# Performance work log

Hardware: AMD Instinct MI355X
Metric: run time of the kernel (lower is better)

Reference implementation:

```python
import jax, jax.numpy as jnp
import numpy as np

B, T, C, H = 2, 2048, 1024, 16
D = C // H  # head_dim = 64


def setup_inputs() -> dict:
    key = jax.random.key(0)
    ks = jax.random.split(key, 5)
    s = 1.0 / np.sqrt(C)
    return {
        "x": jax.random.normal(ks[0], (B, T, C), jnp.float32),
        "Wq": jax.random.normal(ks[1], (C, C), jnp.float32) * s,
        "bq": jnp.zeros((C,), jnp.float32),
        "Wk": jax.random.normal(ks[2], (C, C), jnp.float32) * s,
        "bk": jnp.zeros((C,), jnp.float32),
        "Wv": jax.random.normal(ks[3], (C, C), jnp.float32) * s,
        "bv": jnp.zeros((C,), jnp.float32),
        "Wo": jax.random.normal(ks[4], (C, C), jnp.float32) * s,
        "bo": jnp.zeros((C,), jnp.float32),
    }


def reference(x, Wq, bq, Wk, bk, Wv, bv, Wo, bo):
    Bx, Tx, Cx = x.shape
    # torch Linear: y = x @ W.T + b
    q = (x @ Wq.T + bq).reshape(Bx, Tx, H, D).transpose(0, 2, 1, 3)  # [B,H,T,D]
    k = (x @ Wk.T + bk).reshape(Bx, Tx, H, D).transpose(0, 2, 1, 3)
    v = (x @ Wv.T + bv).reshape(Bx, Tx, H, D).transpose(0, 2, 1, 3)
    att = jnp.einsum("bhqd,bhkd->bhqk", q, k) / np.sqrt(D).astype(np.float32)
    mask = jnp.tril(jnp.ones((Tx, Tx), bool))  # causal mask [T,T]
    att = jnp.where(mask, att, -jnp.inf)
    att = jax.nn.softmax(att, axis=-1)
    out = jnp.einsum("bhqk,bhkd->bhqd", att, v)
    out = out.transpose(0, 2, 1, 3).reshape(Bx, Tx, Cx)
    return out @ Wo.T + bo
```

## Files before the change

### kernel.cpp

```cpp
#include <hip/hip_runtime.h>
#include <hip/hip_bf16.h>

#define B_ 2
#define T_ 2048
#define C_ 1024
#define H_ 16
#define D_ 64

typedef unsigned short u16;
typedef __bf16 bf16x8 __attribute__((ext_vector_type(8)));
typedef float floatx4 __attribute__((ext_vector_type(4)));

__device__ __forceinline__ float bf2f(u16 u) {
  union { unsigned int i; float f; } x; x.i = ((unsigned int)u) << 16; return x.f;
}
__device__ __forceinline__ u16 f2bf(float f) {
  union { float f; unsigned int i; } x; x.f = f;
  unsigned int r = x.i + 0x7fffu + ((x.i >> 16) & 1u);
  return (u16)(r >> 16);
}

__device__ __forceinline__ void gld16(void* lds, const void* g) {
  __builtin_amdgcn_global_load_lds(
      (const __attribute__((address_space(1))) unsigned int*)g,
      (__attribute__((address_space(3))) unsigned int*)lds, 16, 0, 0);
}

#define NXF4 1048576
#define NWF4 262144

__global__ __launch_bounds__(256) void cvt_all(
    const float* __restrict__ x,  const float* __restrict__ Wq,
    const float* __restrict__ Wk, const float* __restrict__ Wv,
    const float* __restrict__ Wo, u16* __restrict__ dst_base)
{
  const int i = blockIdx.x * 256 + threadIdx.x;
  const float* src; size_t off;
  if (i < NXF4)               { src = x;  off = i; }
  else if (i < NXF4 + NWF4)   { src = Wq; off = i - NXF4; }
  else if (i < NXF4 + 2*NWF4) { src = Wk; off = i - (NXF4 + NWF4); }
  else if (i < NXF4 + 3*NWF4) { src = Wv; off = i - (NXF4 + 2*NWF4); }
  else                        { src = Wo; off = i - (NXF4 + 3*NWF4); }
  float4 f = ((const float4*)src)[off];
  ushort4 o;
  o.x = f2bf(f.x); o.y = f2bf(f.y); o.z = f2bf(f.z); o.w = f2bf(f.w);
  ((ushort4*)dst_base)[i] = o;
}

#define QSCALE 0.1803368801111f

#define MFMA16(MH, NH, BREG)                                                  \
  do {                                                                        \
    __builtin_amdgcn_s_setprio(1);                                            \
    _Pragma("unroll")                                                         \
    for (int f = 0; f < 4; ++f) {                                             \
      _Pragma("unroll")                                                       \
      for (int g = 0; g < 2; ++g) {                                           \
        acc[(MH)*4 + f][(NH)*2 + g] = __builtin_amdgcn_mfma_f32_16x16x32_bf16(\
            a[f][0], BREG[g][0], acc[(MH)*4 + f][(NH)*2 + g], 0, 0, 0);       \
        acc[(MH)*4 + f][(NH)*2 + g] = __builtin_amdgcn_mfma_f32_16x16x32_bf16(\
            a[f][1], BREG[g][1], acc[(MH)*4 + f][(NH)*2 + g], 0, 0, 0);       \
      }                                                                       \
    }                                                                         \
    __builtin_amdgcn_s_setprio(0);                                            \
  } while (0)

#define PBAR()                                                \
  do {                                                        \
    asm volatile("" ::: "memory");                            \
    __builtin_amdgcn_s_barrier();                             \
    asm volatile("s_waitcnt lgkmcnt(0)" ::: "memory");        \
  } while (0)

#define EBAR()                                                \
  do {                                                        \
    asm volatile("" ::: "memory");                            \
    __builtin_amdgcn_s_barrier();                             \
    asm volatile("" ::: "memory");                            \
  } while (0)

__global__ __launch_bounds__(512, 2) void gemm_qkv8(
    const u16* __restrict__ X, const u16* __restrict__ Wb,
    const float* __restrict__ b0, const float* __restrict__ b1,
    const float* __restrict__ b2,
    u16* __restrict__ Yq, u16* __restrict__ Yk, u16* __restrict__ Yv)
{
  __shared__ __align__(16) u16 L[65536];

  const int tid  = threadIdx.x;
  const int lane = tid & 63;
  const int m16  = lane & 15;
  const int q4   = lane >> 4;
  const int wv   = tid >> 6;
  const int wm   = wv >> 2;
  const int wn   = wv & 3;

  const int bid = blockIdx.x;
  const int xcd = bid & 7;
  const int idx = bid >> 3;
  const int bx  = (xcd & 3) * 4 + (idx & 3);
  const int by  = (xcd >> 2) * 6 + (idx >> 2);

  const u16* Abase  = X  + (size_t)bx * 256 * C_;
  const u16* Bbase  = Wb + (size_t)by * 256 * C_;
  const u16* A1base = Abase + (size_t)128 * C_;
  const u16* B1base = Bbase + (size_t)128 * C_;

  const int s0 = tid,       r0 = s0 >> 3;
  const int s1 = tid + 512, r1 = s1 >> 3;
  const int k0a = ((s0 & 7) ^ (r0 & 7)) * 8;
  const int k1a = ((s1 & 7) ^ (r1 & 7)) * 8;

#define STAGE(dsthalf, srcrows, kofs)                                         \
  do {                                                                        \
    gld16(&(dsthalf)[s0 * 8], (srcrows) + (size_t)r0 * C_ + (kofs) + k0a);    \
    gld16(&(dsthalf)[s1 * 8], (srcrows) + (size_t)r1 * C_ + (kofs) + k1a);    \
  } while (0)

  u16* buf0 = L;
  u16* buf1 = L + 32768;

  STAGE(buf0 + 16384, Bbase, 0);
  STAGE(buf0,         Abase, 0);
  STAGE(buf0 + 24576, B1base, 0);
  STAGE(buf0 + 8192,  A1base, 0);
  STAGE(buf1 + 16384, Bbase, 64);
  STAGE(buf1,         Abase, 64);
  asm volatile("s_waitcnt vmcnt(4)" ::: "memory");
  __builtin_amdgcn_s_barrier();
  asm volatile("" ::: "memory");

  floatx4 acc[8][4] = {};

  const int a0off = m16 * 64 + ((q4      ^ (lane & 7)) * 8);
  const int a1off = m16 * 64 + (((q4 + 4) ^ (lane & 7)) * 8);
  const int bro   = (wn & 1) * 4096;

  for (int i = 0; i < 16; ++i) {
    u16* buf  = (i & 1) ? buf1 : buf0;
    u16* bufn = (i & 1) ? buf0 : buf1;
    const u16* Ah = buf + wm * 8192;
    const u16* Bh = buf + 16384 + (wn >> 1) * 8192;
    const bool p1 = (i + 1) < 16;
    const bool p2 = (i + 2) < 16;
    const int  k1 = (i + 1) * 64;
    const int  k2 = (i + 2) * 64;

    bf16x8 a[4][2], bA[2][2], bB[2][2];

#pragma unroll
    for (int f = 0; f < 4; ++f) {
      a[f][0] = *(const bf16x8*)&Ah[f * 1024 + a0off];
      a[f][1] = *(const bf16x8*)&Ah[f * 1024 + a1off];
    }
#pragma unroll
    for (int g = 0; g < 2; ++g) {
      bA[g][0] = *(const bf16x8*)&Bh[bro + g * 1024 + a0off];
      bA[g][1] = *(const bf16x8*)&Bh[bro + g * 1024 + a1off];
    }
    if (p1) STAGE(bufn + 24576, B1base, k1);
    PBAR();
    MFMA16(0, 0, bA);
    EBAR();

#pragma unroll
    for (int g = 0; g < 2; ++g) {
      bB[g][0] = *(const bf16x8*)&Bh[bro + 2048 + g * 1024 + a0off];
      bB[g][1] = *(const bf16x8*)&Bh[bro + 2048 + g * 1024 + a1off];
    }
    if (p1) STAGE(bufn + 8192, A1base, k1);
    PBAR();
    MFMA16(0, 1, bB);
    EBAR();

#pragma unroll
    for (int f = 0; f < 4; ++f) {
      a[f][0] = *(const bf16x8*)&Ah[4096 + f * 1024 + a0off];
      a[f][1] = *(const bf16x8*)&Ah[4096 + f * 1024 + a1off];
    }
    if (p2) STAGE(buf + 16384, Bbase, k2);
    PBAR();
    MFMA16(1, 1, bB);
    EBAR();

    if (p2) STAGE(buf, Abase, k2);
    PBAR();
    MFMA16(1, 0, bA);
    asm volatile("" ::: "memory");
    if (p2) asm volatile("s_waitcnt vmcnt(4)" ::: "memory");
    else    asm volatile("s_waitcnt vmcnt(0)" ::: "memory");
    __builtin_amdgcn_s_barrier();
    asm volatile("" ::: "memory");
  }

  const int z    = by >> 2;
  const int nloc = (by & 3) * 256 + wn * 64;
  const float* bias = (z == 0) ? b0 : (z == 1) ? b1 : b2;
  const int mbase = bx * 256 + wm * 128 + q4 * 4;

  if (z == 2) {
#pragma unroll
    for (int nf = 0; nf < 4; ++nf) {
      const int nz = nloc + nf * 16 + m16;
      const float bv = bias[nz];
      const int h = nz >> 6, d = nz & (D_ - 1);
#pragma unroll
      for (int mf = 0; mf < 8; ++mf) {
        const int m  = mbase + mf * 16;
        const int bb = m >> 11, t = m & (T_ - 1);
        ushort4 pk;
        pk.x = f2bf(acc[mf][nf][0] + bv);
        pk.y = f2bf(acc[mf][nf][1] + bv);
        pk.z = f2bf(acc[mf][nf][2] + bv);
        pk.w = f2bf(acc[mf][nf][3] + bv);
        *(ushort4*)&Yv[(((size_t)bb * H_ + h) * D_ + d) * T_ + t] = pk;
      }
    }
  } else {
    u16* Y = z ? Yk : Yq;
    const float sc = z ? 1.0f : QSCALE;
#pragma unroll
    for (int nf = 0; nf < 4; ++nf) {
      const int nz = nloc + nf * 16 + m16;
      const float bv = bias[nz];
      const int h = nz >> 6, d = nz & (D_ - 1);
#pragma unroll
      for (int mf = 0; mf < 8; ++mf) {
        const int m  = mbase + mf * 16;
        const int bb = m >> 11, tq = m & (T_ - 1);
#pragma unroll
        for (int r = 0; r < 4; ++r) {
          Y[(((size_t)bb * H_ + h) * T_ + (tq + r)) * D_ + d] =
              f2bf((acc[mf][nf][r] + bv) * sc);
        }
      }
    }
  }
}

__global__ __launch_bounds__(256) void gemm_out(
    const u16* __restrict__ X, const u16* __restrict__ W,
    const float* __restrict__ bias, float* __restrict__ Yf)
{
  const int K = C_, N = C_;
  __shared__ __align__(16) u16 As[128 * 32];
  __shared__ __align__(16) u16 Bs[64 * 32];

  const int tid  = threadIdx.x;
  const int wv   = tid >> 6;
  const int lane = tid & 63;
  const int mcol = lane & 15;
  const int quad = lane >> 4;
  const int wr = wv >> 1, wc = wv & 1;
  const int m0 = blockIdx.x * 128;
  const int n0 = blockIdx.y * 64;

  const int srow = tid >> 2;
  const int scol = (tid & 3) * 8;
  const u16* xp0 = X + (size_t)(m0 + srow) * K + scol;
  const u16* xp1 = xp0 + (size_t)64 * K;
  const u16* wp  = W + (size_t)(n0 + srow) * K + scol;

  floatx4 acc[4][2] = {};

  for (int k0 = 0; k0 < K; k0 += 32) {
    gld16(&As[tid * 8],        xp0 + k0);
    gld16(&As[2048 + tid * 8], xp1 + k0);
    gld16(&Bs[tid * 8],        wp + k0);
    __syncthreads();

    bf16x8 a[4], b[2];
#pragma unroll
    for (int rf = 0; rf < 4; ++rf)
      a[rf] = *(const bf16x8*)&As[(wr * 64 + rf * 16 + mcol) * 32 + quad * 8];
#pragma unroll
    for (int cf = 0; cf < 2; ++cf)
      b[cf] = *(const bf16x8*)&Bs[(wc * 32 + cf * 16 + mcol) * 32 + quad * 8];
#pragma unroll
    for (int rf = 0; rf < 4; ++rf)
#pragma unroll
      for (int cf = 0; cf < 2; ++cf)
        acc[rf][cf] = __builtin_amdgcn_mfma_f32_16x16x32_bf16(
            a[rf], b[cf], acc[rf][cf], 0, 0, 0);
    __syncthreads();
  }

#pragma unroll
  for (int cf = 0; cf < 2; ++cf) {
    const int n = n0 + wc * 32 + cf * 16 + mcol;
    const float bv = bias[n];
#pragma unroll
    for (int rf = 0; rf < 4; ++rf) {
#pragma unroll
      for (int r = 0; r < 4; ++r) {
        const int m = m0 + wr * 64 + rf * 16 + quad * 4 + r;
        Yf[(size_t)m * N + n] = acc[rf][cf][r] + bv;
      }
    }
  }
}

#define KSB 4096
#define VTB 5120

__global__ __launch_bounds__(256) void attn_flash(
    const u16* __restrict__ Q, const u16* __restrict__ K,
    const u16* __restrict__ Vg, u16* __restrict__ O)
{
  __shared__ __align__(16) u16 Ks[2 * KSB];
  __shared__ __align__(16) u16 Vt[2 * VTB];
  __shared__ __align__(16) u16 Ps[4][16 * 72];

  const int tid  = threadIdx.x;
  const int wv   = tid >> 6;
  const int lane = tid & 63;
  const int mcol = lane & 15;
  const int quad = lane >> 4;

  const int bx = blockIdx.x;
  const int bh = bx & 31;
  const int iq = 31 - (bx >> 5);
  const size_t base  = (size_t)bh * T_ * D_;
  const size_t vbase = (size_t)bh * D_ * T_;
  const int b = bh >> 4, h = bh & (H_ - 1);

  for (int idx = tid; idx < 16 * 64; idx += 256) {
    const u16 val = (idx < 64) ? (u16)0x3F80 : (u16)0;
    Vt[64 * 64 + idx]       = val;
    Vt[VTB + 64 * 64 + idx] = val;
  }

  const int srow = lane >> 3;
  const int sg   = (lane & 7) ^ srow;
  const int c0 = wv * 2, c1 = wv * 2 + 1;
  const int sl0 = (quad ^ (mcol & 7)) * 8;

  const int h3 = mcol >> 3, lo = mcol & 7;
  u16* psw = &Ps[wv][0];
  int colsw[4];
#pragma unroll
  for (int nt = 0; nt < 4; ++nt)
    colsw[nt] = (((nt * 2 + h3) ^ quad) * 8) + lo;
  const int g0 = quad ^ (mcol >> 2);

  const size_t koff0 = base + (size_t)(c0 * 8 + srow) * D_ + sg * 8;
  const size_t koff1 = base + (size_t)(c1 * 8 + srow) * D_ + sg * 8;
  const size_t voff0 = vbase + (size_t)(c0 * 8 + srow) * T_ + sg * 8;
  const size_t voff1 = vbase + (size_t)(c1 * 8 + srow) * T_ + sg * 8;

  const u16* qg = Q + base + (size_t)(iq * 64 + wv * 16 + mcol) * D_ + quad * 8;
  const bf16x8 qf0 = *(const bf16x8*)qg;
  const bf16x8 qf1 = *(const bf16x8*)(qg + 32);

  floatx4 oacc[5] = {};

  __syncthreads();
  gld16(&Ks[c0 * 512 + lane * 8], K  + koff0);
  gld16(&Ks[c1 * 512 + lane * 8], K  + koff1);
  gld16(&Vt[c0 * 512 + lane * 8], Vg + voff0);
  gld16(&Vt[c1 * 512 + lane * 8], Vg + voff1);

  for (int j = 0; j <= iq; ++j) {
    const int cur = j & 1;
    __syncthreads();

    if (j < iq) {
      const int nb = cur ^ 1;
      const size_t kj = (size_t)(j + 1) * 64 * D_;
      const int    vj = (j + 1) * 64;
      gld16(&Ks[nb * KSB + c0 * 512 + lane * 8], K  + koff0 + kj);
      gld16(&Ks[nb * KSB + c1 * 512 + lane * 8], K  + koff1 + kj);
      gld16(&Vt[nb * VTB + c0 * 512 + lane * 8], Vg + voff0 + vj);
      gld16(&Vt[nb * VTB + c1 * 512 + lane * 8], Vg + voff1 + vj);
    }

    const u16* ksb = &Ks[cur * KSB];
    const u16* vtb = &Vt[cur * VTB];

    floatx4 sacc[4] = {};
#pragma unroll
    for (int nt = 0; nt < 4; ++nt) {
      const u16* kr = &ksb[(nt * 16 + mcol) * 64];
      bf16x8 kb0 = *(const bf16x8*)&kr[sl0];
      bf16x8 kb1 = *(const bf16x8*)&kr[sl0 ^ 32];
      sacc[nt] = __builtin_amdgcn_mfma_f32_16x16x32_bf16(qf0, kb0, sacc[nt], 0, 0, 0);
      sacc[nt] = __builtin_amdgcn_mfma_f32_16x16x32_bf16(qf1, kb1, sacc[nt], 0, 0, 0);
    }

    if (j == iq) {
#pragma unroll
      for (int nt = 0; nt < 4; ++nt) {
        const int col = nt * 16 + mcol;
#pragma unroll
        for (int r = 0; r < 4; ++r)
          if (col > wv * 16 + quad * 4 + r) sacc[nt][r] = -1e30f;
      }
    }

#pragma unroll
    for (int nt = 0; nt < 4; ++nt)
#pragma unroll
      for (int r = 0; r < 4; ++r) {
        const float p = exp2f(sacc[nt][r]);
        psw[(quad * 4 + r) * 72 + colsw[nt]] =
            (u16)((__float_as_uint(p) + 0x8000u) >> 16);
      }

    __builtin_amdgcn_wave_barrier();

    bf16x8 pa0 = *(const bf16x8*)&psw[mcol * 72 + g0 * 8];
    bf16x8 pa1 = *(const bf16x8*)&psw[mcol * 72 + g0 * 8 + 32];
#pragma unroll
    for (int dt = 0; dt < 5; ++dt) {
      const u16* vr = &vtb[(dt * 16 + mcol) * 64];
      bf16x8 vb0 = *(const bf16x8*)&vr[sl0];
      bf16x8 vb1 = *(const bf16x8*)&vr[sl0 ^ 32];
      oacc[dt] = __builtin_amdgcn_mfma_f32_16x16x32_bf16(pa0, vb0, oacc[dt], 0, 0, 0);
      oacc[dt] = __builtin_amdgcn_mfma_f32_16x16x32_bf16(pa1, vb1, oacc[dt], 0, 0, 0);
    }
  }

  float invl[4];
#pragma unroll
  for (int r = 0; r < 4; ++r)
    invl[r] = 1.f / __shfl(oacc[4][r], lane & 48);
#pragma unroll
  for (int dt = 0; dt < 4; ++dt) {
    const int c = h * D_ + dt * 16 + mcol;
#pragma unroll
    for (int r = 0; r < 4; ++r) {
      const int t = iq * 64 + wv * 16 + quad * 4 + r;
      O[((size_t)b * T_ + t) * C_ + c] = f2bf(oacc[dt][r] * invl[r]);
    }
  }
}

extern "C" void kernel_launch(void* const* d_in, const int* in_sizes, int n_in,
                              void* d_out, int out_size, void* d_ws, size_t ws_size,
                              hipStream_t stream) {
  const float* x  = (const float*)d_in[0];
  const float* Wq = (const float*)d_in[1];
  const float* bq = (const float*)d_in[2];
  const float* Wk = (const float*)d_in[3];
  const float* bk = (const float*)d_in[4];
  const float* Wv = (const float*)d_in[5];
  const float* bv = (const float*)d_in[6];
  const float* Wo = (const float*)d_in[7];
  const float* bo = (const float*)d_in[8];
  float* out = (float*)d_out;

  const size_t NX = (size_t)B_ * T_ * C_;
  const size_t NW = (size_t)C_ * C_;

  u16* xb  = (u16*)d_ws;
  u16* wqb = xb  + NX;
  u16* wkb = wqb + NW;
  u16* wvb = wkb + NW;
  u16* wob = wvb + NW;
  u16* q   = wob + NW;
  u16* k   = q   + NX;
  u16* v   = k   + NX;
  u16* ctx = v   + NX;

  cvt_all<<<dim3((NXF4 + 4 * NWF4) / 256), 256, 0, stream>>>(x, Wq, Wk, Wv, Wo, xb);

  gemm_qkv8<<<dim3(192), 512, 0, stream>>>(xb, wqb, bq, bk, bv, q, k, v);

  attn_flash<<<dim3(1024), 256, 0, stream>>>(q, k, v, ctx);

  gemm_out<<<dim3(32, 16), 256, 0, stream>>>(ctx, wob, bo, out);
}
```

Before: 187.4 us.

## Transpose S MFMA and build P operand in registers via permlane swaps

Swaps the MFMA operand order so the score tile comes out transposed, then packs the exp2'd probabilities to bf16 with v_cvt_pk_bf16_f32 and rearranges them across lanes with permlane32/16 swaps. This replaces the per-wave LDS scratch buffer, its stores, the wave barrier and the reloads. It also adds an occupancy hint of 4 blocks per SM via launch_bounds and reorders query-tile scheduling to interleave heavy and light causal tiles. The gains depend on the register permutation being correct for the MFMA A-operand layout, and the launch_bounds hint may cause register spills.

```diff
diff --git a/kernel.cpp b/kernel.cpp
--- a/kernel.cpp
+++ b/kernel.cpp
@@ -18,6 +18,12 @@
   union { float f; unsigned int i; } x; x.f = f;
   unsigned int r = x.i + 0x7fffu + ((x.i >> 16) & 1u);
   return (u16)(r >> 16);
+}
+
+__device__ __forceinline__ unsigned cvtpk(float lo, float hi) {
+  unsigned r;
+  asm("v_cvt_pk_bf16_f32 %0, %1, %2" : "=v"(r) : "v"(lo), "v"(hi));
+  return r;
 }
 
 __device__ __forceinline__ void gld16(void* lds, const void* g) {
@@ -303,13 +309,12 @@
 #define KSB 4096
 #define VTB 5120
 
-__global__ __launch_bounds__(256) void attn_flash(
+__global__ __launch_bounds__(256, 4) void attn_flash(
     const u16* __restrict__ Q, const u16* __restrict__ K,
     const u16* __restrict__ Vg, u16* __restrict__ O)
 {
   __shared__ __align__(16) u16 Ks[2 * KSB];
   __shared__ __align__(16) u16 Vt[2 * VTB];
-  __shared__ __align__(16) u16 Ps[4][16 * 72];
 
   const int tid  = threadIdx.x;
   const int wv   = tid >> 6;
@@ -319,7 +324,10 @@
 
   const int bx = blockIdx.x;
   const int bh = bx & 31;
-  const int iq = 31 - (bx >> 5);
+  const int g  = bx >> 5;
+  const int ga = g & 7, gb = g >> 3;
+  const int iq = (gb == 0) ? 31 - ga : (gb == 1) ? 16 + ga
+               : (gb == 2) ? 15 - ga : ga;
   const size_t base  = (size_t)bh * T_ * D_;
   const size_t vbase = (size_t)bh * D_ * T_;
   const int b = bh >> 4, h = bh & (H_ - 1);
@@ -334,14 +342,6 @@
   const int sg   = (lane & 7) ^ srow;
   const int c0 = wv * 2, c1 = wv * 2 + 1;
   const int sl0 = (quad ^ (mcol & 7)) * 8;
-
-  const int h3 = mcol >> 3, lo = mcol & 7;
-  u16* psw = &Ps[wv][0];
-  int colsw[4];
-#pragma unroll
-  for (int nt = 0; nt < 4; ++nt)
-    colsw[nt] = (((nt * 2 + h3) ^ quad) * 8) + lo;
-  const int g0 = quad ^ (mcol >> 2);
 
   const size_t koff0 = base + (size_t)(c0 * 8 + srow) * D_ + sg * 8;
   const size_t koff1 = base + (size_t)(c1 * 8 + srow) * D_ + sg * 8;
@@ -383,33 +383,44 @@
       const u16* kr = &ksb[(nt * 16 + mcol) * 64];
       bf16x8 kb0 = *(const bf16x8*)&kr[sl0];
       bf16x8 kb1 = *(const bf16x8*)&kr[sl0 ^ 32];
-      sacc[nt] = __builtin_amdgcn_mfma_f32_16x16x32_bf16(qf0, kb0, sacc[nt], 0, 0, 0);
-      sacc[nt] = __builtin_amdgcn_mfma_f32_16x16x32_bf16(qf1, kb1, sacc[nt], 0, 0, 0);
+      sacc[nt] = __builtin_amdgcn_mfma_f32_16x16x32_bf16(kb0, qf0, sacc[nt], 0, 0, 0);
+      sacc[nt] = __builtin_amdgcn_mfma_f32_16x16x32_bf16(kb1, qf1, sacc[nt], 0, 0, 0);
     }
 
     if (j == iq) {
+      const int ql = wv * 16 + mcol;
 #pragma unroll
       for (int nt = 0; nt < 4; ++nt) {
-        const int col = nt * 16 + mcol;
 #pragma unroll
         for (int r = 0; r < 4; ++r)
-          if (col > wv * 16 + quad * 4 + r) sacc[nt][r] = -1e30f;
+          if (nt * 16 + quad * 4 + r > ql) sacc[nt][r] = -1e30f;
       }
     }
 
-#pragma unroll
-    for (int nt = 0; nt < 4; ++nt)
-#pragma unroll
-      for (int r = 0; r < 4; ++r) {
-        const float p = exp2f(sacc[nt][r]);
-        psw[(quad * 4 + r) * 72 + colsw[nt]] =
-            (u16)((__float_as_uint(p) + 0x8000u) >> 16);
-      }
-
-    __builtin_amdgcn_wave_barrier();
-
-    bf16x8 pa0 = *(const bf16x8*)&psw[mcol * 72 + g0 * 8];
-    bf16x8 pa1 = *(const bf16x8*)&psw[mcol * 72 + g0 * 8 + 32];
+    unsigned w0[2], w1[2], w2[2], w3[2];
+#pragma unroll
+    for (int i = 0; i < 2; ++i) {
+      w0[i] = cvtpk(exp2f(sacc[0][2*i]), exp2f(sacc[0][2*i+1]));
+      w1[i] = cvtpk(exp2f(sacc[1][2*i]), exp2f(sacc[1][2*i+1]));
+      w2[i] = cvtpk(exp2f(sacc[2][2*i]), exp2f(sacc[2][2*i+1]));
+      w3[i] = cvtpk(exp2f(sacc[3][2*i]), exp2f(sacc[3][2*i+1]));
+    }
+
+    union { unsigned u[4]; bf16x8 v; } pa0u, pa1u;
+#pragma unroll
+    for (int i = 0; i < 2; ++i) {
+      unsigned x = w0[i], y = w1[i];
+      asm("v_permlane32_swap_b32 %0, %1" : "+v"(x), "+v"(y));
+      asm("v_permlane16_swap_b32 %0, %1" : "+v"(x), "+v"(y));
+      pa0u.u[i] = x; pa0u.u[i + 2] = y;
+      unsigned x2 = w2[i], y2 = w3[i];
+      asm("v_permlane32_swap_b32 %0, %1" : "+v"(x2), "+v"(y2));
+      asm("v_permlane16_swap_b32 %0, %1" : "+v"(x2), "+v"(y2));
+      pa1u.u[i] = x2; pa1u.u[i + 2] = y2;
+    }
+    const bf16x8 pa0 = pa0u.v;
+    const bf16x8 pa1 = pa1u.v;
+
 #pragma unroll
     for (int dt = 0; dt < 5; ++dt) {
       const u16* vr = &vtb[(dt * 16 + mcol) * 64];
```

Result: faster. 183.4 us (-2.1%).
